# Kernel tuning notes

Hardware: AMD Instinct MI355X
Metric: run time of the kernel (lower is better)

Reference implementation:

```python
import jax, jax.numpy as jnp
import numpy as np

DIM, HEADS, DH, P, C = 2048, 8, 256, 7, 128
NP = (56 // P) ** 2          # 64 patches
N = NP + 1 + NP              # 65 pos tokens concatenated with 64 patch tokens = 129
PATCH_FEAT = C * P * P       # 6272
LN_EPS = 1e-5


def patchify(x, p):
    # 'b c (h p1) (w p2) -> b (h w) (p1 p2 c)'
    b, c, H, W = x.shape
    h, w = H // p, W // p
    x = x.reshape(b, c, h, p, w, p).transpose(0, 2, 4, 3, 5, 1)
    return x.reshape(b, h * w, p * p * c)


def setup_inputs() -> dict:
    key = jax.random.key(0)
    ks = jax.random.split(key, 16)
    s = 0.02
    d = dict(
        x_q=jax.random.normal(ks[0], (64, C, 56, 56), jnp.float32),
        x_kv=jax.random.normal(ks[1], (64, C, 56, 56), jnp.float32),
        W_ex=jax.random.normal(ks[2], (PATCH_FEAT, DIM), jnp.float32) * s,
        b_ex=jnp.zeros((DIM,), jnp.float32),
        W_en=jax.random.normal(ks[3], (PATCH_FEAT, DIM), jnp.float32) * s,
        b_en=jnp.zeros((DIM,), jnp.float32),
        pos=jax.random.normal(ks[4], (1, NP + 1, DIM), jnp.float32),
        Wq=jax.random.normal(ks[5], (DIM, HEADS * DH), jnp.float32) * s,
        Wk=jax.random.normal(ks[6], (DIM, HEADS * DH), jnp.float32) * s,
        Wv=jax.random.normal(ks[7], (DIM, HEADS * DH), jnp.float32) * s,
        Wo=jax.random.normal(ks[8], (HEADS * DH, DIM), jnp.float32) * s,
        bo=jnp.zeros((DIM,), jnp.float32),
        gamma=jnp.ones((DIM,), jnp.float32),
        beta=jnp.zeros((DIM,), jnp.float32),
        Wh=jax.random.normal(ks[9], (DIM, PATCH_FEAT), jnp.float32) * s,
        bh=jnp.zeros((PATCH_FEAT,), jnp.float32),
        Wm=jax.random.normal(ks[10], (DH, N), jnp.float32) * s,
        bm=jnp.zeros((N,), jnp.float32),
    )
    return d


def reference(x_q, x_kv, W_ex, b_ex, W_en, b_en, pos, Wq, Wk, Wv, Wo, bo,
              gamma, beta, Wh, bh, Wm, bm):
    b = x_q.shape[0]
    scale = DH ** -0.5
    # image embedder: patch embed + concat pos tokens
    tq = patchify(x_q, P) @ W_ex + b_ex                      # [b, 64, DIM]
    tk = patchify(x_kv, P) @ W_en + b_en                     # [b, 64, DIM]
    posb = jnp.broadcast_to(pos, (b, NP + 1, DIM))
    tq = jnp.concatenate([posb, tq], axis=1)                 # [b, N, DIM]
    tk = jnp.concatenate([posb, tk], axis=1)                 # [b, N, DIM]

    def split_heads(t):
        return t.reshape(b, N, HEADS, DH).transpose(0, 2, 1, 3)  # b h n d

    q = split_heads(tq @ Wq)
    k = split_heads(tk @ Wk)
    v = split_heads(tk @ Wv)

    # VAE-style reparameterize: mu=k, logvar=q
    eps = jax.random.normal(jax.random.key(42), k.shape, k.dtype)
    z = k + jnp.exp(0.5 * q) * eps                           # [b, h, n, d]

    # scale + linear remap d -> N, softmax, weighted sum with v
    dots = (z * scale) @ Wm + bm                             # [b, h, n, N]
    attn = jax.nn.softmax(dots, axis=-1)
    out = jnp.einsum('bhij,bhjd->bhid', attn, v)             # [b, h, n, d]
    out = out.transpose(0, 2, 1, 3).reshape(b, N, HEADS * DH)
    out = out @ Wo + bo                                      # [b, N, DIM]

    # mlp head: LayerNorm + Linear (final rearrange-to-image is shape-only, omitted)
    mu = out.mean(-1, keepdims=True)
    var = ((out - mu) ** 2).mean(-1, keepdims=True)
    ln = (out - mu) * jax.lax.rsqrt(var + LN_EPS) * gamma + beta
    head = ln @ Wh + bh                                      # [b, N, 6272]

    qf = q.reshape(b, -1)
    kf = k.reshape(b, -1)
    qn = qf / jnp.linalg.norm(qf, axis=1, keepdims=True)
    kn = kf / jnp.linalg.norm(kf, axis=1, keepdims=True)
    return head, qn, kn
```

## Files before the change

kernel.cpp:

```cpp
#include <hip/hip_runtime.h>


typedef unsigned short u16;
typedef short bf16x8 __attribute__((ext_vector_type(8)));
typedef unsigned short u16x8 __attribute__((ext_vector_type(8)));
typedef float f32x4 __attribute__((ext_vector_type(4)));

#define WAITV(N) asm volatile("s_waitcnt vmcnt(" #N ")" ::: "memory")

static __device__ __forceinline__ void barx() {
    asm volatile("" ::: "memory");
    __builtin_amdgcn_s_barrier();
    asm volatile("" ::: "memory");
}

static __device__ __forceinline__ u16 f2b(float f) {
    union { float f; unsigned int u; } cv; cv.f = f;
    unsigned int u = cv.u;
    unsigned int lsb = (u >> 16) & 1u;
    u += 0x7fffu + lsb;
    return (u16)(u >> 16);
}

static __device__ __forceinline__ float b2f(u16 u) {
    union { unsigned int i; float f; } c; c.i = ((unsigned int)u) << 16; return c.f;
}

static __device__ __forceinline__ void gemm8p_body(
    const u16* __restrict__ A, const u16* __restrict__ Bt, void* __restrict__ Cv,
    const float* __restrict__ bias, int M, int N, int K,
    int lda, int ldb, int ldc, float alpha, int c_bf16, int row_remap,
    int m0, int n0, u16* lds)
{
    const int tid = threadIdx.x, lane = tid & 63, wave = tid >> 6;
    const int wm = wave >> 2, wn = wave & 3;
    const int l15 = lane & 15, l4 = lane >> 4;
    const int scol = (((lane & 3) ^ ((lane >> 3) & 3)) << 3);
    const int bswz = ((l4 ^ ((l15 >> 1) & 3)) << 3);

    f32x4 acc[8][4] = {};
    const int nt = K >> 6;
    const int niter = nt >> 1;

    auto STAGE = [&](int tt, int kh, int isB) {
        const int c = tt & 1;
        const int k0 = (tt << 6) + (kh << 5);
        const int rbase = isB ? n0 : m0;
        const u16* P = isB ? Bt : A;
        const int ld = isB ? ldb : lda;
        const int lim = isB ? N : M;
        const int dbase = c * 32768 + isB * 16384 + kh * 8192;
        #pragma unroll
        for (int j = 0; j < 2; ++j) {
            const int r0 = j * 128 + wave * 16;
            int g = rbase + r0 + (lane >> 2); g = g < lim ? g : lim - 1;
            const u16* src = P + (long)g * ld + k0 + scol;
            __builtin_amdgcn_global_load_lds(
                (const __attribute__((address_space(1))) void*)src,
                (__attribute__((address_space(3))) void*)&lds[dbase + r0 * 32],
                16, 0, 0);
        }
    };

    bf16x8 bfr[4];
    auto LOADB = [&](int c, int kk) {
        #pragma unroll
        for (int nn = 0; nn < 4; ++nn) {
            const int row = wn * 64 + nn * 16 + l15;
            bfr[nn] = *(const bf16x8*)&lds[c * 32768 + 16384 + kk * 8192 + row * 32 + bswz];
        }
    };
    auto LDA = [&](int c, int kk, int mh, bf16x8* af) {
        #pragma unroll
        for (int mm = 0; mm < 4; ++mm) {
            const int row = wm * 128 + mh * 64 + mm * 16 + l15;
            af[mm] = *(const bf16x8*)&lds[c * 32768 + kk * 8192 + row * 32 + bswz];
        }
    };
    auto MM = [&](const bf16x8* af, int mh) {
        __builtin_amdgcn_s_setprio(1);
        #pragma unroll
        for (int mm = 0; mm < 4; ++mm)
            #pragma unroll
            for (int nn = 0; nn < 4; ++nn)
                acc[mh * 4 + mm][nn] = __builtin_amdgcn_mfma_f32_16x16x32_bf16(
                    af[mm], bfr[nn], acc[mh * 4 + mm][nn], 0, 0, 0);
        __builtin_amdgcn_s_setprio(0);
    };

    STAGE(0, 0, 0); STAGE(0, 0, 1); STAGE(0, 1, 0); STAGE(0, 1, 1);
    STAGE(1, 0, 0); STAGE(1, 0, 1);

    bf16x8 a0[4], a1[4];
    for (int i = 0; i < niter; ++i) {
        const int t0 = 2 * i, t1 = t0 + 1;
        const bool has2 = (t0 + 2 < nt);
        STAGE(t1, 1, 0); WAITV(8);
        barx(); LOADB(0, 0); LDA(0, 0, 0, a0); MM(a0, 0); LDA(0, 0, 1, a1); barx();
        STAGE(t1, 1, 1);
        barx(); MM(a1, 1); barx();
        if (has2) STAGE(t0 + 2, 0, 0);
        WAITV(8);
        barx(); LOADB(0, 1); LDA(0, 1, 0, a0); MM(a0, 0); LDA(0, 1, 1, a1); barx();
        if (has2) STAGE(t0 + 2, 0, 1);
        barx(); MM(a1, 1); barx();
        if (has2) { STAGE(t0 + 2, 1, 0); WAITV(8); } else { WAITV(4); }
        barx(); LOADB(1, 0); LDA(1, 0, 0, a0); MM(a0, 0); LDA(1, 0, 1, a1); barx();
        if (has2) STAGE(t0 + 2, 1, 1);
        barx(); MM(a1, 1); barx();
        if (has2) { STAGE(t1 + 2, 0, 0); WAITV(8); } else { WAITV(0); }
        barx(); LOADB(1, 1); LDA(1, 1, 0, a0); MM(a0, 0); LDA(1, 1, 1, a1); barx();
        if (has2) STAGE(t1 + 2, 0, 1);
        barx(); MM(a1, 1); barx();
    }

    #pragma unroll
    for (int mr = 0; mr < 8; ++mr) {
        #pragma unroll
        for (int nn = 0; nn < 4; ++nn) {
            const int col = n0 + wn * 64 + nn * 16 + l15;
            if (col >= N) continue;
            const float bv = bias ? bias[col] : 0.0f;
            #pragma unroll
            for (int jj = 0; jj < 4; ++jj) {
                const int row = m0 + wm * 128 + mr * 16 + l4 * 4 + jj;
                if (row >= M) continue;
                float v = alpha * acc[mr][nn][jj] + bv;
                long crow = row;
                if (row_remap) crow = (long)(row >> 6) * 129 + 65 + (row & 63);
                if (c_bf16) ((u16*)Cv)[crow * (long)ldc + col] = f2b(v);
                else        ((float*)Cv)[crow * (long)ldc + col] = v;
            }
        }
    }
}

static __device__ __forceinline__ void xcd_swz(int& bx, int& by) {
    const int nbx = gridDim.x, nwg = nbx * gridDim.y;
    const int orig = blockIdx.y * nbx + blockIdx.x;
    const int q8 = nwg >> 3, r8 = nwg & 7;
    const int xcd = orig & 7, sidx = orig >> 3;
    const int wgid = (xcd < r8 ? xcd * (q8 + 1) : r8 * (q8 + 1) + (xcd - r8) * q8) + sidx;
    bx = wgid % nbx; by = wgid / nbx;
}

__global__ __launch_bounds__(512, 2) void gemm_8p(
    const u16* __restrict__ A, const u16* __restrict__ Bt, void* __restrict__ Cv,
    const float* __restrict__ bias, int M, int N, int K,
    int lda, int ldb, int ldc, float alpha, int c_bf16, int row_remap)
{
    __shared__ u16 lds[65536];
    int bx, by; xcd_swz(bx, by);
    gemm8p_body(A, Bt, Cv, bias, M, N, K, lda, ldb, ldc, alpha, c_bf16, row_remap,
                bx * 256, by * 256, lds);
}

__global__ __launch_bounds__(512, 2) void gemm_8p3(
    const u16* A0, const u16* A1, const u16* A2,
    const u16* B0, const u16* B1, const u16* B2,
    u16* C0, u16* C1, u16* C2,
    const float* bias0, const float* bias1, const float* bias2,
    int M, int N, int K, int lda, int ldb, int ldc, float alpha, int row_remap)
{
    __shared__ u16 lds[65536];
    int bx, by; xcd_swz(bx, by);
    const int z = blockIdx.z;
    const u16* A = z == 0 ? A0 : (z == 1 ? A1 : A2);
    const u16* B = z == 0 ? B0 : (z == 1 ? B1 : B2);
    u16* C = z == 0 ? C0 : (z == 1 ? C1 : C2);
    const float* bias = z == 0 ? bias0 : (z == 1 ? bias1 : bias2);
    gemm8p_body(A, B, C, bias, M, N, K, lda, ldb, ldc, alpha, 1, row_remap,
                bx * 256, by * 256, lds);
}

__global__ __launch_bounds__(256, 2) void gemm_pipe(
    const u16* __restrict__ A, const u16* __restrict__ Bt, void* __restrict__ Cv,
    const float* __restrict__ bias, int M, int N, int K,
    int lda, int ldb, int ldc, float alpha, int c_bf16, int row_remap)
{
    __shared__ u16 lds[2 * 16384];

    int bx, by; xcd_swz(bx, by);
    const int m0 = bx * 128, n0 = by * 128;

    const int tid = threadIdx.x, lane = tid & 63, wave = tid >> 6;
    const int wm = wave >> 1, wn = wave & 1;
    const int l15 = lane & 15, l4 = lane >> 4;

    const int srow = tid >> 3;
    const int scol = (((tid & 7) * 16) ^ (((tid >> 3) & 7) << 4)) >> 1;
    const int cf0 = (((0 * 64) + l4 * 16) ^ ((l15 & 7) << 4)) >> 1;
    const int cf1 = (((1 * 64) + l4 * 16) ^ ((l15 & 7) << 4)) >> 1;

    f32x4 acc[4][4] = {};
    const int nt = K >> 6;

    auto STAGE = [&](int c, int t) {
        const int k0 = t << 6;
        #pragma unroll
        for (int j = 0; j < 4; ++j) {
            const int r = j * 32 + srow;
            int ga = m0 + r; ga = ga < M ? ga : M - 1;
            const u16* srcA = A + (long)ga * lda + k0 + scol;
            __builtin_amdgcn_global_load_lds(
                (const __attribute__((address_space(1))) void*)srcA,
                (__attribute__((address_space(3))) void*)&lds[c * 16384 + j * 2048 + wave * 512],
                16, 0, 0);
            int gb = n0 + r; gb = gb < N ? gb : N - 1;
            const u16* srcB = Bt + (long)gb * ldb + k0 + scol;
            __builtin_amdgcn_global_load_lds(
                (const __attribute__((address_space(1))) void*)srcB,
                (__attribute__((address_space(3))) void*)&lds[c * 16384 + 8192 + j * 2048 + wave * 512],
                16, 0, 0);
        }
    };

    STAGE(0, 0);
    __syncthreads();
    for (int t = 0; t < nt; ++t) {
        const int c = t & 1;
        if (t + 1 < nt) STAGE(c ^ 1, t + 1);
        const int ab = c * 16384, bb = ab + 8192;
        #pragma unroll
        for (int kk = 0; kk < 2; ++kk) {
            const int cf = kk ? cf1 : cf0;
            bf16x8 af[4], bfr[4];
            #pragma unroll
            for (int m = 0; m < 4; ++m)
                af[m] = *(const bf16x8*)&lds[ab + (wm * 64 + m * 16 + l15) * 64 + cf];
            #pragma unroll
            for (int n = 0; n < 4; ++n)
                bfr[n] = *(const bf16x8*)&lds[bb + (wn * 64 + n * 16 + l15) * 64 + cf];
            __builtin_amdgcn_s_setprio(1);
            #pragma unroll
            for (int m = 0; m < 4; ++m)
                #pragma unroll
                for (int n = 0; n < 4; ++n)
                    acc[m][n] = __builtin_amdgcn_mfma_f32_16x16x32_bf16(
                        af[m], bfr[n], acc[m][n], 0, 0, 0);
            __builtin_amdgcn_s_setprio(0);
        }
        __syncthreads();
    }

    #pragma unroll
    for (int m = 0; m < 4; ++m) {
        #pragma unroll
        for (int n = 0; n < 4; ++n) {
            const int col = n0 + wn * 64 + n * 16 + l15;
            if (col >= N) continue;
            const float bv = bias ? bias[col] : 0.0f;
            #pragma unroll
            for (int j = 0; j < 4; ++j) {
                const int row = m0 + wm * 64 + m * 16 + l4 * 4 + j;
                if (row >= M) continue;
                float v = alpha * acc[m][n][j] + bv;
                long crow = row;
                if (row_remap) crow = (long)(row >> 6) * 129 + 65 + (row & 63);
                if (c_bf16) ((u16*)Cv)[crow * (long)ldc + col] = f2b(v);
                else        ((float*)Cv)[crow * (long)ldc + col] = v;
            }
        }
    }
}

__global__ __launch_bounds__(256) void gemm_bt(
    const u16* __restrict__ A, const u16* __restrict__ Bt, void* __restrict__ Cv,
    const float* __restrict__ bias, int M, int N, int K,
    int lda, int ldb, int ldc, float alpha, int c_bf16, int row_remap,
    long sA, long sB, long sCo, long sCi, int binner)
{
    const int bz = blockIdx.z;
    const u16* Ab = A + (long)bz * sA;
    const u16* Bb = Bt + (long)bz * sB;
    const long cOff = (long)(bz / binner) * sCo + (long)(bz % binner) * sCi;

    __shared__ u16 As[128][72];
    __shared__ u16 Bs[128][72];

    const int tid = threadIdx.x;
    const int lane = tid & 63;
    const int wave = tid >> 6;
    const int wr = wave >> 1, wc = wave & 1;
    const int l15 = lane & 15, l4 = lane >> 4;
    const int m0 = blockIdx.x * 128, n0 = blockIdx.y * 128;

    const int r = tid >> 3;
    const int kof = (tid & 7) * 8;

    f32x4 acc[4][4] = {};

    const int ktiles = (K + 63) / 64;
    for (int kt = 0; kt < ktiles; ++kt) {
        const int k0 = kt * 64;
        __syncthreads();
        #pragma unroll
        for (int i = 0; i < 4; ++i) {
            const int row = r + 32 * i;
            const int gk = k0 + kof;
            u16x8 v = {0,0,0,0,0,0,0,0};
            const int grow = m0 + row;
            if (grow < M && gk < K)
                v = *(const u16x8*)(Ab + (long)grow * lda + gk);
            *(u16x8*)&As[row][kof] = v;
        }
        #pragma unroll
        for (int i = 0; i < 4; ++i) {
            const int row = r + 32 * i;
            const int gk = k0 + kof;
            u16x8 v = {0,0,0,0,0,0,0,0};
            const int gcol = n0 + row;
            if (gcol < N && gk < K)
                v = *(const u16x8*)(Bb + (long)gcol * ldb + gk);
            *(u16x8*)&Bs[row][kof] = v;
        }
        __syncthreads();
        #pragma unroll
        for (int ks = 0; ks < 2; ++ks) {
            bf16x8 af[4], bfr[4];
            #pragma unroll
            for (int m = 0; m < 4; ++m)
                af[m] = *(const bf16x8*)&As[wr*64 + m*16 + l15][ks*32 + l4*8];
            #pragma unroll
            for (int n = 0; n < 4; ++n)
                bfr[n] = *(const bf16x8*)&Bs[wc*64 + n*16 + l15][ks*32 + l4*8];
            #pragma unroll
            for (int m = 0; m < 4; ++m)
                #pragma unroll
                for (int n = 0; n < 4; ++n)
                    acc[m][n] = __builtin_amdgcn_mfma_f32_16x16x32_bf16(
                        af[m], bfr[n], acc[m][n], 0, 0, 0);
        }
    }

    #pragma unroll
    for (int m = 0; m < 4; ++m) {
        #pragma unroll
        for (int n = 0; n < 4; ++n) {
            const int col = n0 + wc*64 + n*16 + l15;
            if (col >= N) continue;
            const float bv = bias ? bias[col] : 0.0f;
            #pragma unroll
            for (int j = 0; j < 4; ++j) {
                const int row = m0 + wr*64 + m*16 + l4*4 + j;
                if (row >= M) continue;
                float v = alpha * acc[m][n][j] + bv;
                long crow = row;
                if (row_remap) crow = (long)(row >> 6) * 129 + 65 + (row & 63);
                if (c_bf16) ((u16*)Cv)[cOff + crow * (long)ldc + col] = f2b(v);
                else        ((float*)Cv)[cOff + crow * (long)ldc + col] = v;
            }
        }
    }
}

__global__ __launch_bounds__(256, 2) void fdots_kernel(
    const u16* __restrict__ z, const u16* __restrict__ Wm_t,
    const float* __restrict__ bm, u16* __restrict__ attn)
{
    __shared__ u16 wlds[144 * 264];
    const int tid = threadIdx.x;
    for (int i = tid; i < 144 * 32; i += 256) {
        const int row = i >> 5, c8 = i & 31;
        *(u16x8*)&wlds[row * 264 + c8 * 8] = *(const u16x8*)&Wm_t[row * 256 + c8 * 8];
    }
    __syncthreads();
    const int lane = tid & 63, wave = tid >> 6;
    const int l15 = lane & 15, l4 = lane >> 4;
    const long rowbase = (long)blockIdx.x * 128 + wave * 32;

    f32x4 acc[2][9] = {};
    #pragma unroll
    for (int kk = 0; kk < 8; ++kk) {
        bf16x8 af[2];
        #pragma unroll
        for (int rg = 0; rg < 2; ++rg)
            af[rg] = *(const bf16x8*)&z[(rowbase + rg * 16 + l15) * 256 + kk * 32 + l4 * 8];
        #pragma unroll
        for (int c = 0; c < 9; ++c) {
            const bf16x8 bf = *(const bf16x8*)&wlds[(c * 16 + l15) * 264 + kk * 32 + l4 * 8];
            #pragma unroll
            for (int rg = 0; rg < 2; ++rg)
                acc[rg][c] = __builtin_amdgcn_mfma_f32_16x16x32_bf16(af[rg], bf, acc[rg][c], 0, 0, 0);
        }
    }

    float bmv[9];
    #pragma unroll
    for (int c = 0; c < 9; ++c) {
        const int col = c * 16 + l15;
        bmv[c] = (col < 129) ? bm[col] : 0.0f;
    }

    #pragma unroll
    for (int rg = 0; rg < 2; ++rg) {
        #pragma unroll
        for (int j = 0; j < 4; ++j) {
            float v[9]; float mx = -1e30f;
            #pragma unroll
            for (int c = 0; c < 9; ++c) {
                const int col = c * 16 + l15;
                v[c] = (col < 129) ? (0.0625f * acc[rg][c][j] + bmv[c]) : -1e30f;
                mx = fmaxf(mx, v[c]);
            }
            #pragma unroll
            for (int o = 1; o < 16; o <<= 1) mx = fmaxf(mx, __shfl_xor(mx, o, 64));
            float s = 0.f;
            #pragma unroll
            for (int c = 0; c < 9; ++c) {
                v[c] = (c * 16 + l15 < 129) ? expf(v[c] - mx) : 0.0f;
                s += v[c];
            }
            #pragma unroll
            for (int o = 1; o < 16; o <<= 1) s += __shfl_xor(s, o, 64);
            const float inv = 1.0f / s;
            u16* ar = attn + (rowbase + rg * 16 + l4 * 4 + j) * 144;
            #pragma unroll
            for (int c = 0; c < 9; ++c)
                ar[c * 16 + l15] = f2b(v[c] * inv);
        }
    }
}

__global__ __launch_bounds__(256) void row128_kernel(
    const u16* __restrict__ attn, const u16* __restrict__ v_t, u16* __restrict__ outm)
{
    const int bh = blockIdx.x, d = threadIdx.x;
    const int b = bh >> 3, h = bh & 7;
    __shared__ float a[144];
    for (int j = threadIdx.x; j < 144; j += 256)
        a[j] = (j < 129) ? b2f(attn[((long)bh * 129 + 128) * 144 + j]) : 0.0f;
    __syncthreads();
    const u16* vr = v_t + ((long)bh * 256 + d) * 144;
    float s = 0.f;
    #pragma unroll
    for (int j8 = 0; j8 < 18; ++j8) {
        const bf16x8 vv = *(const bf16x8*)&vr[j8 * 8];
        #pragma unroll
        for (int e = 0; e < 8; ++e) s += a[j8 * 8 + e] * b2f((u16)vv[e]);
    }
    outm[((long)(b * 129 + 128)) * 2048 + h * 256 + d] = f2b(s);
}

__global__ __launch_bounds__(256) void transpose_conv4(
    const float* in0, const float* in1, const float* in2, const float* in3,
    u16* o0, u16* o1, u16* o2, u16* o3, int K, int N, int KP, int NPd)
{
    const int zz = blockIdx.z;
    const float* in = zz == 0 ? in0 : (zz == 1 ? in1 : (zz == 2 ? in2 : in3));
    u16* out = zz == 0 ? o0 : (zz == 1 ? o1 : (zz == 2 ? o2 : o3));
    __shared__ float tile[32][33];
    const int k0 = blockIdx.x * 32, n0 = blockIdx.y * 32;
    const int tx = threadIdx.x, ty = threadIdx.y;
    #pragma unroll
    for (int i = 0; i < 4; ++i) {
        const int k = k0 + ty + i*8, n = n0 + tx;
        tile[ty + i*8][tx] = (k < K && n < N) ? in[(long)k * N + n] : 0.0f;
    }
    __syncthreads();
    #pragma unroll
    for (int i = 0; i < 4; ++i) {
        const int n = n0 + ty + i*8, k = k0 + tx;
        if (n < NPd && k < KP) out[(long)n * KP + k] = f2b(tile[tx][ty + i*8]);
    }
}

__global__ __launch_bounds__(256) void patchify_kernel(
    const float* __restrict__ xq, const float* __restrict__ xkv,
    u16* __restrict__ oq, u16* __restrict__ okv)
{
    __shared__ u16 tile[64 * 7 * 58];
    const int zz = blockIdx.z;
    const float* x = (zz >= 64) ? xkv : xq;
    u16* out = (zz >= 64) ? okv : oq;
    const int b = zz & 63, hh = blockIdx.y, cg = blockIdx.x;
    const int c0 = cg * 64;
    for (int i = threadIdx.x; i < 64 * 392; i += 256) {
        const int c = i / 392, rem = i - c * 392;
        const int p1 = rem / 56, w = rem - p1 * 56;
        const float v = x[(((long)b * 128 + c0 + c) * 56 + hh * 7 + p1) * 56 + w];
        tile[(c * 7 + p1) * 58 + w] = f2b(v);
    }
    __syncthreads();
    #pragma unroll
    for (int ww = 0; ww < 8; ++ww) {
        const long base = ((long)(b * 64 + hh * 8 + ww)) * 6272 + c0;
        for (int j = threadIdx.x; j < 49 * 64; j += 256) {
            const int c = j & 63, pp = j >> 6;
            const int p1 = pp / 7, p2 = pp - p1 * 7;
            out[base + pp * 128 + c] = tile[(c * 7 + p1) * 58 + ww * 7 + p2];
        }
    }
}

__global__ __launch_bounds__(256) void posfill_kernel(
    const float* __restrict__ pos, u16* __restrict__ Tq, u16* __restrict__ Tk)
{
    const int col = blockIdx.x * 256 + threadIdx.x;
    const int t = blockIdx.y, b = blockIdx.z;
    const u16 v = f2b(pos[(long)t * 2048 + col]);
    const long idx = ((long)b * 129 + t) * 2048 + col;
    Tq[idx] = v; Tk[idx] = v;
}

__global__ void vtrans_kernel(const u16* __restrict__ vmat, u16* __restrict__ v_t)
{
    const int bh = blockIdx.z; const int b = bh >> 3, h = bh & 7;
    const int d0 = blockIdx.x * 32, n0 = blockIdx.y * 32;
    __shared__ u16 tile[32][33];
    const int tx = threadIdx.x, ty = threadIdx.y;
    #pragma unroll
    for (int i = 0; i < 4; ++i) {
        const int n = n0 + ty + i*8;
        if (n < 129)
            tile[ty + i*8][tx] = vmat[((long)b*129 + n) * 2048 + h*256 + d0 + tx];
    }
    __syncthreads();
    #pragma unroll
    for (int i = 0; i < 4; ++i) {
        const int d = d0 + ty + i*8, n = n0 + tx;
        if (n < 144)
            v_t[((long)bh * 256 + d) * 144 + n] = (n < 129) ? tile[tx][ty + i*8] : (u16)0;
    }
}

static __device__ __forceinline__ unsigned int rotl32(unsigned int x, int d) {
    return (x << d) | (x >> (32 - d));
}

static __device__ __forceinline__ float threefry_normal(unsigned int i) {
    const unsigned int ks0 = 0u, ks1 = 42u;
    const unsigned int ks2 = ks0 ^ ks1 ^ 0x1BD11BDAu;
    unsigned int x0 = 0u + ks0;
    unsigned int x1 = i + ks1;
#define TF_R(rr) { x0 += x1; x1 = rotl32(x1, rr); x1 ^= x0; }
    TF_R(13) TF_R(15) TF_R(26) TF_R(6)
    x0 += ks1; x1 += ks2 + 1u;
    TF_R(17) TF_R(29) TF_R(16) TF_R(24)
    x0 += ks2; x1 += ks0 + 2u;
    TF_R(13) TF_R(15) TF_R(26) TF_R(6)
    x0 += ks0; x1 += ks1 + 3u;
    TF_R(17) TF_R(29) TF_R(16) TF_R(24)
    x0 += ks1; x1 += ks2 + 4u;
    TF_R(13) TF_R(15) TF_R(26) TF_R(6)
    x0 += ks2; x1 += ks0 + 5u;
#undef TF_R
    const unsigned int bits = x0 ^ x1;
    const unsigned int fb = (bits >> 9) | 0x3f800000u;
    union { unsigned int u; float f; } cv; cv.u = fb;
    const float f = cv.f - 1.0f;
    const float lo = -0.99999994f;
    float u = f * (1.0f - lo) + lo;
    u = fmaxf(lo, u);
    return 1.4142135623730951f * erfinvf(u);
}

__global__ __launch_bounds__(256) void z_kernel(
    const u16* __restrict__ qmat, const u16* __restrict__ kmat,
    const float* __restrict__ norms, u16* __restrict__ z,
    float* __restrict__ outq, float* __restrict__ outk)
{
    const unsigned int i = blockIdx.x * 256u + threadIdx.x;
    const int d = i & 255; const unsigned int t = i >> 8;
    const int n = t % 129; const int bh = t / 129;
    const int b = bh >> 3, h = bh & 7;
    const long src = ((long)(b * 129 + n)) * 2048 + h * 256 + d;
    const float qf = b2f(qmat[src]);
    const float kf = b2f(kmat[src]);
    const float eps = threefry_normal(i);
    z[i] = f2b(kf + expf(0.5f * qf) * eps);
    outq[i] = qf / norms[b];
    outk[i] = kf / norms[64 + b];
}

__global__ __launch_bounds__(256) void ln_kernel(
    const float* __restrict__ proj, const float* __restrict__ gamma,
    const float* __restrict__ beta, u16* __restrict__ ln)
{
    const int row = blockIdx.x;
    const float* p = proj + (long)row * 2048;
    const int tid = threadIdx.x;
    float v[8]; float s = 0.f, s2 = 0.f;
    #pragma unroll
    for (int i = 0; i < 8; ++i) {
        v[i] = p[tid + i * 256]; s += v[i]; s2 += v[i] * v[i];
    }
    #pragma unroll
    for (int o = 32; o > 0; o >>= 1) { s += __shfl_down(s, o, 64); s2 += __shfl_down(s2, o, 64); }
    __shared__ float sh[8];
    if ((tid & 63) == 0) { sh[tid >> 6] = s; sh[4 + (tid >> 6)] = s2; }
    __syncthreads();
    s = sh[0] + sh[1] + sh[2] + sh[3];
    s2 = sh[4] + sh[5] + sh[6] + sh[7];
    const float mu = s * (1.0f / 2048.0f);
    const float var = s2 * (1.0f / 2048.0f) - mu * mu;
    const float rinv = 1.0f / sqrtf(var + 1e-5f);
    u16* lr = ln + (long)row * 2048;
    #pragma unroll
    for (int i = 0; i < 8; ++i) {
        const int c = tid + i * 256;
        lr[c] = f2b((v[i] - mu) * rinv * gamma[c] + beta[c]);
    }
}

__global__ __launch_bounds__(256) void norm_reduce(
    const u16* __restrict__ qmat, const u16* __restrict__ kmat, float* __restrict__ norms)
{
    const int b = blockIdx.x & 63;
    const u16* src = (blockIdx.x >= 64 ? kmat : qmat) + (long)b * 264192;
    float s = 0.f;
    for (int i = threadIdx.x; i < 264192; i += 256) { const float x = b2f(src[i]); s += x * x; }
    #pragma unroll
    for (int o = 32; o > 0; o >>= 1) s += __shfl_down(s, o, 64);
    __shared__ float sh[4];
    if ((threadIdx.x & 63) == 0) sh[threadIdx.x >> 6] = s;
    __syncthreads();
    if (threadIdx.x == 0) norms[blockIdx.x] = sqrtf(sh[0] + sh[1] + sh[2] + sh[3]);
}

extern "C" void kernel_launch(void* const* d_in, const int* in_sizes, int n_in,
                              void* d_out, int out_size, void* d_ws, size_t ws_size,
                              hipStream_t stream)
{
    const float* x_q   = (const float*)d_in[0];
    const float* x_kv  = (const float*)d_in[1];
    const float* W_ex  = (const float*)d_in[2];
    const float* b_ex  = (const float*)d_in[3];
    const float* W_en  = (const float*)d_in[4];
    const float* b_en  = (const float*)d_in[5];
    const float* pos   = (const float*)d_in[6];
    const float* Wq    = (const float*)d_in[7];
    const float* Wk    = (const float*)d_in[8];
    const float* Wv    = (const float*)d_in[9];
    const float* Wo    = (const float*)d_in[10];
    const float* bo    = (const float*)d_in[11];
    const float* gamma = (const float*)d_in[12];
    const float* beta  = (const float*)d_in[13];
    const float* Wh    = (const float*)d_in[14];
    const float* bh    = (const float*)d_in[15];
    const float* Wm    = (const float*)d_in[16];
    const float* bm    = (const float*)d_in[17];
    (void)in_sizes; (void)n_in; (void)out_size; (void)ws_size;

    char* ws = (char*)d_ws;
    size_t off = 0;
    auto alloc = [&](size_t bytes) -> char* {
        char* p = ws + off;
        off += (bytes + 255) & ~(size_t)255;
        return p;
    };
    u16*   Xq_p  = (u16*)alloc(4096UL * 6272 * 2);
    u16*   Xk_p  = (u16*)alloc(4096UL * 6272 * 2);
    u16*   Wex_t = (u16*)alloc(2048UL * 6272 * 2);
    u16*   Wen_t = (u16*)alloc(2048UL * 6272 * 2);
    u16*   Tq    = (u16*)alloc(8256UL * 2048 * 2);
    u16*   Tk    = (u16*)alloc(8256UL * 2048 * 2);
    u16*   Wq_t  = (u16*)alloc(2048UL * 2048 * 2);
    u16*   Wk_t  = (u16*)alloc(2048UL * 2048 * 2);
    u16*   Wv_t  = (u16*)alloc(2048UL * 2048 * 2);
    u16*   qmat  = (u16*)alloc(8256UL * 2048 * 2);
    u16*   kmat  = (u16*)alloc(8256UL * 2048 * 2);
    u16*   vmat  = (u16*)alloc(8256UL * 2048 * 2);
    u16*   v_t   = (u16*)alloc(512UL * 256 * 144 * 2);
    u16*   z     = (u16*)alloc(66048UL * 256 * 2);
    u16*   attn  = (u16*)alloc(66048UL * 144 * 2);
    u16*   outm  = (u16*)alloc(8256UL * 2048 * 2);
    float* proj  = (float*)alloc(8256UL * 2048 * 4);
    u16*   ln    = (u16*)alloc(8256UL * 2048 * 2);
    u16*   Wo_t  = (u16*)alloc(2048UL * 2048 * 2);
    u16*   Wh_t  = (u16*)alloc(6272UL * 2048 * 2);
    u16*   Wm_t  = (u16*)alloc(144UL * 256 * 2);
    float* norms = (float*)alloc(128UL * 4);

    transpose_conv4<<<dim3(196, 64, 2), dim3(32, 8), 0, stream>>>(
        W_ex, W_en, W_ex, W_en, Wex_t, Wen_t, Wex_t, Wen_t, 6272, 2048, 6272, 2048);
    patchify_kernel<<<dim3(2, 8, 128), 256, 0, stream>>>(x_q, x_kv, Xq_p, Xk_p);
    posfill_kernel<<<dim3(8, 65, 64), 256, 0, stream>>>(pos, Tq, Tk);

    gemm_8p3<<<dim3(16, 8, 2), 512, 0, stream>>>(
        Xq_p, Xk_p, Xk_p, Wex_t, Wen_t, Wen_t, Tq, Tk, Tk,
        b_ex, b_en, b_en, 4096, 2048, 6272, 6272, 6272, 2048, 1.0f, 1);

    transpose_conv4<<<dim3(64, 64, 4), dim3(32, 8), 0, stream>>>(
        Wq, Wk, Wv, Wo, Wq_t, Wk_t, Wv_t, Wo_t, 2048, 2048, 2048, 2048);
    gemm_8p3<<<dim3(33, 8, 3), 512, 0, stream>>>(
        Tq, Tk, Tk, Wq_t, Wk_t, Wv_t, qmat, kmat, vmat,
        nullptr, nullptr, nullptr, 8256, 2048, 2048, 2048, 2048, 2048, 1.0f, 0);

    vtrans_kernel<<<dim3(8, 5, 512), dim3(32, 8), 0, stream>>>(vmat, v_t);

    norm_reduce<<<128, 256, 0, stream>>>(qmat, kmat, norms);
    {
        float* outq = (float*)d_out + 51781632L;
        float* outk = outq + 16908288L;
        z_kernel<<<66048, 256, 0, stream>>>(qmat, kmat, norms, z, outq, outk);
    }

    transpose_conv4<<<dim3(8, 5, 1), dim3(32, 8), 0, stream>>>(
        Wm, Wm, Wm, Wm, Wm_t, Wm_t, Wm_t, Wm_t, 256, 129, 256, 144);
    fdots_kernel<<<516, 256, 0, stream>>>(z, Wm_t, bm, attn);

    {
        dim3 grid(1, 2, 512);
        gemm_bt<<<grid, 256, 0, stream>>>(attn, v_t, outm, nullptr,
            128, 256, 144, 144, 144, 2048, 1.0f, 1, 0,
            129L * 144, 256L * 144, 129L * 2048, 256L, 8);
    }
    row128_kernel<<<512, 256, 0, stream>>>(attn, v_t, outm);

    gemm_pipe<<<dim3(65, 16), 256, 0, stream>>>(
        outm, Wo_t, proj, bo, 8256, 2048, 2048, 2048, 2048, 2048, 1.0f, 0, 0);

    ln_kernel<<<8256, 256, 0, stream>>>(proj, gamma, beta, ln);

    transpose_conv4<<<dim3(64, 196, 1), dim3(32, 8), 0, stream>>>(
        Wh, Wh, Wh, Wh, Wh_t, Wh_t, Wh_t, Wh_t, 2048, 6272, 2048, 6272);
    gemm_8p<<<dim3(33, 25), 512, 0, stream>>>(
        ln, Wh_t, (float*)d_out, bh, 8256, 6272, 2048, 2048, 2048, 6272, 1.0f, 0, 0);
}
```

Before: 1.628 ms.

## Reschedule GEMM main loop with one barrier per k-phase

Restructures the bf16 MFMA GEMM main loop so each k-phase has a single wait plus barrier instead of four barriers. Both halves of the next global-to-LDS stage are issued together, right after the current fragments are read from LDS, so they overlap with the two MFMA groups. The goal is to cut barrier stalls and give loads and math more room to overlap. The risk is an LDS write-after-read race: correctness now relies on the single barrier per phase and the vmcnt counts still ordering buffer reuse.

Result: no change. 1.614 ms (-0.9%).

```diff
diff --git a/kernel.cpp b/kernel.cpp
--- a/kernel.cpp
+++ b/kernel.cpp
@@ -95,23 +95,24 @@
     for (int i = 0; i < niter; ++i) {
         const int t0 = 2 * i, t1 = t0 + 1;
         const bool has2 = (t0 + 2 < nt);
-        STAGE(t1, 1, 0); WAITV(8);
-        barx(); LOADB(0, 0); LDA(0, 0, 0, a0); MM(a0, 0); LDA(0, 0, 1, a1); barx();
-        STAGE(t1, 1, 1);
-        barx(); MM(a1, 1); barx();
-        if (has2) STAGE(t0 + 2, 0, 0);
-        WAITV(8);
-        barx(); LOADB(0, 1); LDA(0, 1, 0, a0); MM(a0, 0); LDA(0, 1, 1, a1); barx();
-        if (has2) STAGE(t0 + 2, 0, 1);
-        barx(); MM(a1, 1); barx();
-        if (has2) { STAGE(t0 + 2, 1, 0); WAITV(8); } else { WAITV(4); }
-        barx(); LOADB(1, 0); LDA(1, 0, 0, a0); MM(a0, 0); LDA(1, 0, 1, a1); barx();
-        if (has2) STAGE(t0 + 2, 1, 1);
-        barx(); MM(a1, 1); barx();
-        if (has2) { STAGE(t1 + 2, 0, 0); WAITV(8); } else { WAITV(0); }
-        barx(); LOADB(1, 1); LDA(1, 1, 0, a0); MM(a0, 0); LDA(1, 1, 1, a1); barx();
-        if (has2) STAGE(t1 + 2, 0, 1);
-        barx(); MM(a1, 1); barx();
+        WAITV(8); barx();
+        LOADB(0, 0); LDA(0, 0, 0, a0);
+        STAGE(t1, 1, 0); STAGE(t1, 1, 1);
+        MM(a0, 0); LDA(0, 0, 1, a1); MM(a1, 1);
+        WAITV(8); barx();
+        LOADB(0, 1); LDA(0, 1, 0, a0);
+        if (has2) { STAGE(t0 + 2, 0, 0); STAGE(t0 + 2, 0, 1); }
+        MM(a0, 0); LDA(0, 1, 1, a1); MM(a1, 1);
+        if (has2) { WAITV(8); } else { WAITV(4); }
+        barx();
+        LOADB(1, 0); LDA(1, 0, 0, a0);
+        if (has2) { STAGE(t0 + 2, 1, 0); STAGE(t0 + 2, 1, 1); }
+        MM(a0, 0); LDA(1, 0, 1, a1); MM(a1, 1);
+        if (has2) { WAITV(8); } else { WAITV(0); }
+        barx();
+        LOADB(1, 1); LDA(1, 1, 0, a0);
+        if (has2) { STAGE(t1 + 2, 0, 0); STAGE(t1 + 2, 0, 1); }
+        MM(a0, 0); LDA(1, 1, 1, a1); MM(a1, 1);
     }
 
     #pragma unroll
```
